# Optimization experiments

Measured on AMD Instinct MI355X. Metric: run time of the kernel, lower is better.

Reference implementation:

```python
import jax, jax.numpy as jnp
import numpy as np

N = 50000
E = 800000
IN_DIM = 128
HID = 64
HEADS = 4
OUT_DIM = 121
NEG_SLOPE = 0.2
EPS = 1e-16


def setup_inputs() -> dict:
    key = jax.random.key(0)
    ks = jax.random.split(key, 16)
    glorot = lambda k, shape: jax.random.normal(k, shape, jnp.float32) * (2.0 / (shape[0] + shape[-1])) ** 0.5
    HC = HEADS * HID
    return {
        "x": jax.random.normal(ks[0], (N, IN_DIM), jnp.float32),
        "edge_index": jax.random.randint(ks[1], (2, E), 0, N, jnp.int64),
        # conv1: GATConv(IN_DIM -> HID, heads=HEADS, concat)
        "W1": glorot(ks[2], (IN_DIM, HC)),
        "att_src1": glorot(ks[3], (HEADS, HID)),
        "att_dst1": glorot(ks[4], (HEADS, HID)),
        "b1": jnp.zeros((HC,), jnp.float32),
        # conv2: GATConv(HC -> HID, heads=HEADS, concat)
        "W2": glorot(ks[5], (HC, HC)),
        "att_src2": glorot(ks[6], (HEADS, HID)),
        "att_dst2": glorot(ks[7], (HEADS, HID)),
        "b2": jnp.zeros((HC,), jnp.float32),
        # post_mp: Linear(HC, HID) -> Dropout -> Linear(HID, OUT_DIM)
        "Wm1": glorot(ks[8], (HC, HID)),
        "bm1": jnp.zeros((HID,), jnp.float32),
        "Wm2": glorot(ks[9], (HID, OUT_DIM)),
        "bm2": jnp.zeros((OUT_DIM,), jnp.float32),
    }


def gat_conv(x, src, dst, W, att_src, att_dst, b):
    """PyG GATConv (concat=True, add_self_loops already applied to src/dst)."""
    n = x.shape[0]
    h = (x @ W).reshape(n, HEADS, -1)                     # [N, H, C]
    a_s = jnp.einsum("nhc,hc->nh", h, att_src)            # [N, H]
    a_d = jnp.einsum("nhc,hc->nh", h, att_dst)            # [N, H]
    e = jax.nn.leaky_relu(a_s[src] + a_d[dst], NEG_SLOPE)  # [Etot, H]
    # segment softmax over destination nodes
    m = jax.ops.segment_max(e, dst, num_segments=n)       # [N, H]
    ex = jnp.exp(e - m[dst])
    denom = jax.ops.segment_sum(ex, dst, num_segments=n)  # [N, H]
    alpha = ex / (denom[dst] + EPS)                        # [Etot, H]
    out = jax.ops.segment_sum(alpha[:, :, None] * h[src], dst, num_segments=n)  # [N, H, C]
    return out.reshape(n, -1) + b


def reference(x, edge_index, W1, att_src1, att_dst1, b1, W2, att_src2, att_dst2, b2, Wm1, bm1, Wm2, bm2):
    n = x.shape[0]
    loops = jnp.arange(n, dtype=edge_index.dtype)
    src = jnp.concatenate([edge_index[0], loops])
    dst = jnp.concatenate([edge_index[1], loops])
    h = jax.nn.relu(gat_conv(x, src, dst, W1, att_src1, att_dst1, b1))
    h = jax.nn.relu(gat_conv(h, src, dst, W2, att_src2, att_dst2, b2))
    h = h @ Wm1 + bm1
    h = h @ Wm2 + bm2
    return jax.nn.sigmoid(h)
```

## Files before the change

kernel.cpp:

```cpp
#include <hip/hip_runtime.h>
#include <hip/hip_bf16.h>
#include <float.h>

#define HEADS 4
#define HID 64
#define HC 256
#define NEG_SLOPE 0.2f
#define EPS 1e-16f
#define SLOG 7
#define SLOTS 128

typedef short bf16x8 __attribute__((ext_vector_type(8)));
typedef float f32x4 __attribute__((ext_vector_type(4)));
typedef unsigned short ushort8 __attribute__((ext_vector_type(8)));

__device__ __forceinline__ float bflo(unsigned u) { return __uint_as_float(u << 16); }
__device__ __forceinline__ float bfhi(unsigned u) { return __uint_as_float(u & 0xffff0000u); }
__device__ __forceinline__ unsigned packbf2(float a, float b) {
  __hip_bfloat16 ha = __float2bfloat16(a), hb = __float2bfloat16(b);
  unsigned short ua = *reinterpret_cast<unsigned short*>(&ha);
  unsigned short ub = *reinterpret_cast<unsigned short*>(&hb);
  return (unsigned)ua | ((unsigned)ub << 16);
}

#define PK 40

__global__ void __launch_bounds__(256) conv_gemm_attn(
    const __hip_bfloat16* __restrict__ A, const __hip_bfloat16* __restrict__ Bt,
    __hip_bfloat16* __restrict__ Cb,
    const float* __restrict__ att_s, const float* __restrict__ att_d,
    float* __restrict__ a_s, float* __restrict__ a_d,
    float* __restrict__ blockmax, int M, int K) {
  __shared__ unsigned short As[2][64 * PK];
  __shared__ unsigned short Bs[2][256 * PK];
  int tid = threadIdx.x;
  int lane = tid & 63, w = tid >> 6;
  int col16 = lane & 15, quad = lane >> 4;
  int row0 = blockIdx.x * 64;
  const unsigned short* Ag = (const unsigned short*)A;
  const unsigned short* Bg = (const unsigned short*)Bt;

  int ar = tid >> 2;
  int ako = (tid & 3) << 3;
  int agr = row0 + ar; if (agr >= M) agr = M - 1;
  const unsigned short* aga = Ag + (size_t)agr * K + ako;

  f32x4 acc[4][4] = {};
  int niter = K >> 5;

  ushort8 pa, pb[4];
  pa = *(const ushort8*)(aga);
#pragma unroll
  for (int p = 0; p < 4; p++) {
    int i2 = tid + (p << 8);
    int br = i2 >> 2, bko = (i2 & 3) << 3;
    pb[p] = *(const ushort8*)(Bg + (size_t)br * K + bko);
  }
  *(ushort8*)(&As[0][ar * PK + ako]) = pa;
#pragma unroll
  for (int p = 0; p < 4; p++) {
    int i2 = tid + (p << 8);
    int br = i2 >> 2, bko = (i2 & 3) << 3;
    *(ushort8*)(&Bs[0][br * PK + bko]) = pb[p];
  }
  __syncthreads();

  for (int it = 0; it < niter; ++it) {
    int cur = it & 1, nxt = cur ^ 1;
    int k1 = (it + 1) << 5;
    if (it + 1 < niter) {
      pa = *(const ushort8*)(aga + k1);
#pragma unroll
      for (int p = 0; p < 4; p++) {
        int i2 = tid + (p << 8);
        int br = i2 >> 2, bko = (i2 & 3) << 3;
        pb[p] = *(const ushort8*)(Bg + (size_t)br * K + k1 + bko);
      }
    }
    bf16x8 a[4], b[4];
#pragma unroll
    for (int i = 0; i < 4; i++)
      a[i] = *(const bf16x8*)(&As[cur][(i * 16 + col16) * PK + quad * 8]);
#pragma unroll
    for (int j = 0; j < 4; j++)
      b[j] = *(const bf16x8*)(&Bs[cur][((w << 6) + j * 16 + col16) * PK + quad * 8]);
#pragma unroll
    for (int i = 0; i < 4; i++)
#pragma unroll
      for (int j = 0; j < 4; j++)
        acc[i][j] = __builtin_amdgcn_mfma_f32_16x16x32_bf16(a[i], b[j], acc[i][j], 0, 0, 0);
    if (it + 1 < niter) {
      *(ushort8*)(&As[nxt][ar * PK + ako]) = pa;
#pragma unroll
      for (int p = 0; p < 4; p++) {
        int i2 = tid + (p << 8);
        int br = i2 >> 2, bko = (i2 & 3) << 3;
        *(ushort8*)(&Bs[nxt][br * PK + bko]) = pb[p];
      }
    }
    __syncthreads();
  }

#pragma unroll
  for (int i = 0; i < 4; i++) {
#pragma unroll
    for (int j = 0; j < 4; j++) {
      int gc = (w << 6) + j * 16 + col16;
      int grb = row0 + i * 16 + quad * 4;
#pragma unroll
      for (int r = 0; r < 4; r++) {
        int gr = grb + r;
        if (gr < M) Cb[(size_t)gr * 256 + gc] = __float2bfloat16(acc[i][j][r]);
      }
    }
  }

  float ws4[4], wd4[4];
#pragma unroll
  for (int j = 0; j < 4; j++) {
    ws4[j] = att_s[(w << 6) + j * 16 + col16];
    wd4[j] = att_d[(w << 6) + j * 16 + col16];
  }
  float wavemax = -FLT_MAX;
#pragma unroll
  for (int i = 0; i < 4; i++) {
#pragma unroll
    for (int r = 0; r < 4; r++) {
      float vs = 0.f, vd = 0.f;
#pragma unroll
      for (int j = 0; j < 4; j++) {
        vs += acc[i][j][r] * ws4[j];
        vd += acc[i][j][r] * wd4[j];
      }
#pragma unroll
      for (int off = 1; off < 16; off <<= 1) {
        vs += __shfl_xor(vs, off);
        vd += __shfl_xor(vd, off);
      }
      int gr = row0 + i * 16 + quad * 4 + r;
      if (col16 == 0 && gr < M) {
        a_s[(size_t)gr * 4 + w] = vs;
        a_d[(size_t)gr * 4 + w] = vd;
      }
      wavemax = fmaxf(wavemax, vs);
    }
  }
  wavemax = fmaxf(wavemax, __shfl_xor(wavemax, 16));
  wavemax = fmaxf(wavemax, __shfl_xor(wavemax, 32));
  if (lane == 0) blockmax[(size_t)blockIdx.x * 4 + w] = wavemax;
}

__global__ void __launch_bounds__(256) reduce_gmax(const float* __restrict__ blockmax,
                                                   float* __restrict__ gmaxf, int goff, int nb) {
  __shared__ float wm[4][4];
  int tid = threadIdx.x, lane = tid & 63, w = tid >> 6;
  int hd = tid & 3;
  float m = -FLT_MAX;
  for (int i = tid >> 2; i < nb; i += 64)
    m = fmaxf(m, blockmax[(size_t)i * 4 + hd]);
#pragma unroll
  for (int off = 4; off < 64; off <<= 1)
    m = fmaxf(m, __shfl_xor(m, off));
  if (lane < 4) wm[w][lane] = m;
  __syncthreads();
  if (tid < 4) {
    float r = fmaxf(fmaxf(wm[0][tid], wm[1][tid]), fmaxf(wm[2][tid], wm[3][tid]));
    gmaxf[goff + tid] = r;
  }
}

#define TS 72

__global__ void __launch_bounds__(256) postmp_fused(
    const __hip_bfloat16* __restrict__ A, const __hip_bfloat16* __restrict__ Wm1t,
    const __hip_bfloat16* __restrict__ Wm2t, const float* __restrict__ bm1,
    const float* __restrict__ bm2, float* __restrict__ out, int M) {
  __shared__ unsigned short smem[24576];
  unsigned short* W2s = &smem[15360];
  int tid = threadIdx.x;
  int lane = tid & 63, w = tid >> 6;
  int col16 = lane & 15, quad = lane >> 4;
  int row0 = blockIdx.x * 128;
  const unsigned short* Ag = (const unsigned short*)A;
  const unsigned short* Bg = (const unsigned short*)Wm1t;
  const unsigned short* W2g = (const unsigned short*)Wm2t;

#pragma unroll
  for (int c = tid; c < 1024; c += 256) {
    int r = c >> 3, ko = (c & 7) << 3;
    ushort8 v = {};
    if (r < 121) v = *(const ushort8*)(W2g + (size_t)r * 64 + ko);
    *(ushort8*)(&W2s[r * TS + ko]) = v;
  }

  int ar0 = tid >> 2, ako = (tid & 3) << 3;
  int agr0 = row0 + ar0;       if (agr0 >= M) agr0 = M - 1;
  int agr1 = row0 + ar0 + 64;  if (agr1 >= M) agr1 = M - 1;
  const unsigned short* aga0 = Ag + (size_t)agr0 * 256 + ako;
  const unsigned short* aga1 = Ag + (size_t)agr1 * 256 + ako;
  int br = tid >> 2, bko = (tid & 3) << 3;
  const unsigned short* bga = Bg + (size_t)br * 256 + bko;

  f32x4 acc1[2][4] = {};
  ushort8 pa0, pa1, pbv;
  pa0 = *(const ushort8*)(aga0);
  pa1 = *(const ushort8*)(aga1);
  pbv = *(const ushort8*)(bga);
  *(ushort8*)(&smem[ar0 * PK + ako]) = pa0;
  *(ushort8*)(&smem[(ar0 + 64) * PK + ako]) = pa1;
  *(ushort8*)(&smem[10240 + br * PK + bko]) = pbv;
  __syncthreads();

  for (int it = 0; it < 8; ++it) {
    int cur = it & 1, nxt = cur ^ 1;
    unsigned short* Asc = &smem[cur * 5120];
    unsigned short* Bsc = &smem[10240 + cur * 2560];
    int k1 = (it + 1) << 5;
    if (it + 1 < 8) {
      pa0 = *(const ushort8*)(aga0 + k1);
      pa1 = *(const ushort8*)(aga1 + k1);
      pbv = *(const ushort8*)(bga + k1);
    }
    bf16x8 a[2], b[4];
#pragma unroll
    for (int i = 0; i < 2; i++)
      a[i] = *(const bf16x8*)(&Asc[(w * 32 + i * 16 + col16) * PK + quad * 8]);
#pragma unroll
    for (int j = 0; j < 4; j++)
      b[j] = *(const bf16x8*)(&Bsc[(j * 16 + col16) * PK + quad * 8]);
#pragma unroll
    for (int i = 0; i < 2; i++)
#pragma unroll
      for (int j = 0; j < 4; j++)
        acc1[i][j] = __builtin_amdgcn_mfma_f32_16x16x32_bf16(a[i], b[j], acc1[i][j], 0, 0, 0);
    if (it + 1 < 8) {
      unsigned short* Asn = &smem[nxt * 5120];
      unsigned short* Bsn = &smem[10240 + nxt * 2560];
      *(ushort8*)(&Asn[ar0 * PK + ako]) = pa0;
      *(ushort8*)(&Asn[(ar0 + 64) * PK + ako]) = pa1;
      *(ushort8*)(&Bsn[br * PK + bko]) = pbv;
    }
    __syncthreads();
  }

  unsigned short* T = &smem[0];
#pragma unroll
  for (int i = 0; i < 2; i++) {
#pragma unroll
    for (int j = 0; j < 4; j++) {
      int col = j * 16 + col16;
      float bv = bm1[col];
#pragma unroll
      for (int r = 0; r < 4; r++) {
        int rl = w * 32 + i * 16 + quad * 4 + r;
        __hip_bfloat16 hv = __float2bfloat16(acc1[i][j][r] + bv);
        T[rl * TS + col] = *reinterpret_cast<unsigned short*>(&hv);
      }
    }
  }
  __syncthreads();

  int wm2 = w & 1, wn2 = w >> 1;
  f32x4 acc2[4][4] = {};
#pragma unroll
  for (int kk = 0; kk < 2; kk++) {
    bf16x8 a[4], b[4];
#pragma unroll
    for (int i = 0; i < 4; i++)
      a[i] = *(const bf16x8*)(&T[(wm2 * 64 + i * 16 + col16) * TS + kk * 32 + quad * 8]);
#pragma unroll
    for (int j = 0; j < 4; j++)
      b[j] = *(const bf16x8*)(&W2s[(wn2 * 64 + j * 16 + col16) * TS + kk * 32 + quad * 8]);
#pragma unroll
    for (int i = 0; i < 4; i++)
#pragma unroll
      for (int j = 0; j < 4; j++)
        acc2[i][j] = __builtin_amdgcn_mfma_f32_16x16x32_bf16(a[i], b[j], acc2[i][j], 0, 0, 0);
  }
#pragma unroll
  for (int i = 0; i < 4; i++) {
#pragma unroll
    for (int j = 0; j < 4; j++) {
      int gc = wn2 * 64 + j * 16 + col16;
      if (gc >= 121) continue;
      float bv = bm2[gc];
      int grb = row0 + wm2 * 64 + i * 16 + quad * 4;
#pragma unroll
      for (int r = 0; r < 4; r++) {
        int gr = grb + r;
        if (gr >= M) continue;
        float v = acc2[i][j][r] + bv;
        out[(size_t)gr * 121 + gc] = 1.f / (1.f + __expf(-v));
      }
    }
  }
}

__global__ void setup_all(const float* __restrict__ x, __hip_bfloat16* __restrict__ xb,
                          const float* __restrict__ W1, const float* __restrict__ W2,
                          const float* __restrict__ Wm1, const float* __restrict__ Wm2,
                          __hip_bfloat16* __restrict__ W1t, __hip_bfloat16* __restrict__ W2t,
                          __hip_bfloat16* __restrict__ Wm1t, __hip_bfloat16* __restrict__ Wm2t,
                          int* __restrict__ cur, int* __restrict__ slots,
                          int n, int castBlocks, int prepBlocks) {
  int b = blockIdx.x;
  int tid = threadIdx.x;
  if (b < castBlocks) {
    int i = b * 256 + tid;
    if (i < n * 32) {
      float4 v = *(const float4*)(x + 4 * (size_t)i);
      uint2 pk;
      pk.x = packbf2(v.x, v.y);
      pk.y = packbf2(v.z, v.w);
      *(uint2*)((unsigned*)xb + 2 * (size_t)i) = pk;
    }
    return;
  }
  b -= castBlocks;
  if (b < prepBlocks) {
    int i = b * 256 + tid;
    if (i < 128 * 256) {
      int nn = i / 128, kk = i - nn * 128;
      W1t[i] = __float2bfloat16(W1[(size_t)kk * 256 + nn]);
      return;
    }
    i -= 128 * 256;
    if (i < 256 * 256) {
      int nn = i / 256, kk = i - nn * 256;
      W2t[i] = __float2bfloat16(W2[(size_t)kk * 256 + nn]);
      return;
    }
    i -= 256 * 256;
    if (i < 256 * 64) {
      int nn = i / 256, kk = i - nn * 256;
      Wm1t[i] = __float2bfloat16(Wm1[(size_t)kk * 64 + nn]);
      return;
    }
    i -= 256 * 64;
    if (i < 64 * 121) {
      int nn = i / 64, kk = i - nn * 64;
      Wm2t[i] = __float2bfloat16(Wm2[(size_t)kk * 121 + nn]);
    }
    return;
  }
  b -= prepBlocks;
  {
    int i = b * 256 + tid;
    if (i < n) {
      cur[i] = 1;
      slots[(size_t)i << SLOG] = i;
    }
  }
}

__global__ void slot_fill(const int* __restrict__ ei, int E,
                          int* __restrict__ cur, int* __restrict__ slots) {
  int i = blockIdx.x * 256 + threadIdx.x;
  if (i >= E) return;
  int s = ei[i], d = ei[E + i];
  int pos = atomicAdd(&cur[d], 1);
  slots[((size_t)d << SLOG) + pos] = s;
}

__global__ void __launch_bounds__(256) gat_aggregate(
    const __hip_bfloat16* __restrict__ hb, const float* __restrict__ a_src,
    const float* __restrict__ a_dst, const int* __restrict__ cnt_arr,
    const int* __restrict__ slots, const float* __restrict__ bias,
    const float* __restrict__ gmaxf, int goff,
    __hip_bfloat16* __restrict__ out, int n) {
  __shared__ float plds[4][256];
  int wid = threadIdx.x >> 6;
  int lane = threadIdx.x & 63;
  int half = lane >> 5;
  int l32 = lane & 31;
  int qh = l32 >> 3;
  int node = (blockIdx.x << 2) + wid;
  if (node >= n) return;
  float4 adv = *(const float4*)(a_dst + (size_t)node * 4);
  float m0 = gmaxf[goff + 0] + adv.x; m0 = fmaxf(m0, NEG_SLOPE * m0);
  float m1 = gmaxf[goff + 1] + adv.y; m1 = fmaxf(m1, NEG_SLOPE * m1);
  float m2 = gmaxf[goff + 2] + adv.z; m2 = fmaxf(m2, NEG_SLOPE * m2);
  float m3 = gmaxf[goff + 3] + adv.w; m3 = fmaxf(m3, NEG_SLOPE * m3);
  int cntN = __builtin_amdgcn_readfirstlane(cnt_arr[node]);
  int beg = node << SLOG;
  const uint4* hw4 = (const uint4*)hb;

  float lq = 0.f;
  float c0 = 0.f, c1 = 0.f, c2 = 0.f, c3 = 0.f;
  float c4 = 0.f, c5 = 0.f, c6 = 0.f, c7 = 0.f;

  for (int cbeg = 0; cbeg < cntN; cbeg += 64) {
    int cnt = cntN - cbeg; if (cnt > 64) cnt = 64;
    int eidx = beg + cbeg + (lane < cnt ? lane : cnt - 1);
    int s_l = slots[eidx];
    float4 as = *(const float4*)(a_src + (size_t)s_l * 4);
    float v0 = as.x + adv.x; v0 = fmaxf(v0, NEG_SLOPE * v0);
    float v1 = as.y + adv.y; v1 = fmaxf(v1, NEG_SLOPE * v1);
    float v2 = as.z + adv.z; v2 = fmaxf(v2, NEG_SLOPE * v2);
    float v3 = as.w + adv.w; v3 = fmaxf(v3, NEG_SLOPE * v3);
    float p0 = __expf(v0 - m0), p1 = __expf(v1 - m1);
    float p2 = __expf(v2 - m2), p3 = __expf(v3 - m3);
    *(float4*)&plds[wid][lane * 4] = make_float4(p0, p1, p2, p3);
    __builtin_amdgcn_s_waitcnt(0);

    auto step = [&](int j) {
      int jj = j + half;
      bool dup = jj >= cnt;
      int jc = dup ? cnt - 1 : jj;
      int sj = __shfl(s_l, jc);
      float pq = plds[wid][jc * 4 + qh];
      if (dup) pq = 0.f;
      uint4 d = hw4[(size_t)sj * 32 + l32];
      c0 += pq * bflo(d.x); c1 += pq * bfhi(d.x);
      c2 += pq * bflo(d.y); c3 += pq * bfhi(d.y);
      c4 += pq * bflo(d.z); c5 += pq * bfhi(d.z);
      c6 += pq * bflo(d.w); c7 += pq * bfhi(d.w);
      lq += pq;
    };
    int j = 0;
    for (; j + 8 <= cnt; j += 8) { step(j); step(j + 2); step(j + 4); step(j + 6); }
    for (; j < cnt; j += 2) step(j);
  }

  lq += __shfl_xor(lq, 32);
  c0 += __shfl_xor(c0, 32); c1 += __shfl_xor(c1, 32);
  c2 += __shfl_xor(c2, 32); c3 += __shfl_xor(c3, 32);
  c4 += __shfl_xor(c4, 32); c5 += __shfl_xor(c5, 32);
  c6 += __shfl_xor(c6, 32); c7 += __shfl_xor(c7, 32);

  if (half == 0) {
    float4 bA = *(const float4*)(bias + 8 * l32);
    float4 bB = *(const float4*)(bias + 8 * l32 + 4);
    float rq = 1.f / (lq + EPS);
    float o0 = fmaxf(c0 * rq + bA.x, 0.f);
    float o1 = fmaxf(c1 * rq + bA.y, 0.f);
    float o2 = fmaxf(c2 * rq + bA.z, 0.f);
    float o3 = fmaxf(c3 * rq + bA.w, 0.f);
    float o4 = fmaxf(c4 * rq + bB.x, 0.f);
    float o5 = fmaxf(c5 * rq + bB.y, 0.f);
    float o6 = fmaxf(c6 * rq + bB.z, 0.f);
    float o7 = fmaxf(c7 * rq + bB.w, 0.f);
    uint4 pk;
    pk.x = packbf2(o0, o1);
    pk.y = packbf2(o2, o3);
    pk.z = packbf2(o4, o5);
    pk.w = packbf2(o6, o7);
    *(uint4*)((unsigned*)out + (size_t)node * 128 + l32 * 4) = pk;
  }
}

extern "C" void kernel_launch(void* const* d_in, const int* in_sizes, int n_in,
                              void* d_out, int out_size, void* d_ws, size_t ws_size,
                              hipStream_t stream) {
  const float* x      = (const float*)d_in[0];
  const int*   ei     = (const int*)d_in[1];
  const float* W1     = (const float*)d_in[2];
  const float* att_s1 = (const float*)d_in[3];
  const float* att_d1 = (const float*)d_in[4];
  const float* b1     = (const float*)d_in[5];
  const float* W2     = (const float*)d_in[6];
  const float* att_s2 = (const float*)d_in[7];
  const float* att_d2 = (const float*)d_in[8];
  const float* b2     = (const float*)d_in[9];
  const float* Wm1    = (const float*)d_in[10];
  const float* bm1    = (const float*)d_in[11];
  const float* Wm2    = (const float*)d_in[12];
  const float* bm2    = (const float*)d_in[13];
  float* out = (float*)d_out;

  int n = in_sizes[0] / 128;
  int E = in_sizes[1] / 2;

  char* ws = (char*)d_ws;
  size_t off = 0;
  auto carve = [&](size_t bytes) {
    char* p = ws + off;
    off += (bytes + 255) & ~(size_t)255;
    return p;
  };
  __hip_bfloat16* hb   = (__hip_bfloat16*)carve((size_t)n * HC * 2);
  __hip_bfloat16* aggb = (__hip_bfloat16*)carve((size_t)n * HC * 2);
  __hip_bfloat16* xb   = (__hip_bfloat16*)carve((size_t)n * 128 * 2);
  __hip_bfloat16* W1t  = (__hip_bfloat16*)carve((size_t)128 * HC * 2);
  __hip_bfloat16* W2t  = (__hip_bfloat16*)carve((size_t)HC * HC * 2);
  __hip_bfloat16* Wm1t = (__hip_bfloat16*)carve((size_t)HC * HID * 2);
  __hip_bfloat16* Wm2t = (__hip_bfloat16*)carve((size_t)HID * 121 * 2);
  float* as    = (float*)carve((size_t)n * HEADS * 4);
  float* ad    = (float*)carve((size_t)n * HEADS * 4);
  int*   cur   = (int*)carve((size_t)n * 4);
  int*   slots = (int*)carve(((size_t)n << SLOG) * 4);
  float* blockmax = (float*)carve((size_t)((n + 63) / 64) * 4 * 4);
  float* gmaxf    = (float*)carve((size_t)8 * 4);
  (void)ws_size;

  int rows64 = (n + 63) / 64;
  int castBlocks = (n * 32 + 255) / 256;
  int prepBlocks = (122432 + 255) / 256;
  int slotBlocks = (n + 255) / 256;

  setup_all<<<castBlocks + prepBlocks + slotBlocks, 256, 0, stream>>>(
      x, xb, W1, W2, Wm1, Wm2, W1t, W2t, Wm1t, Wm2t, cur, slots,
      n, castBlocks, prepBlocks);
  slot_fill<<<(E + 255) / 256, 256, 0, stream>>>(ei, E, cur, slots);

  conv_gemm_attn<<<rows64, 256, 0, stream>>>(
      xb, W1t, hb, att_s1, att_d1, as, ad, blockmax, n, 128);
  reduce_gmax<<<1, 256, 0, stream>>>(blockmax, gmaxf, 0, rows64);
  gat_aggregate<<<(n + 3) / 4, 256, 0, stream>>>(hb, as, ad, cur, slots, b1, gmaxf, 0, aggb, n);

  conv_gemm_attn<<<rows64, 256, 0, stream>>>(
      aggb, W2t, hb, att_s2, att_d2, as, ad, blockmax, n, HC);
  reduce_gmax<<<1, 256, 0, stream>>>(blockmax, gmaxf, 4, rows64);
  gat_aggregate<<<(n + 3) / 4, 256, 0, stream>>>(hb, as, ad, cur, slots, b2, gmaxf, 4, aggb, n);

  postmp_fused<<<(n + 127) / 128, 256, 0, stream>>>(aggb, Wm1t, Wm2t, bm1, bm2, out, n);
}
```

Baseline: 363.2 us.

## Fuse fp32-to-bf16 input cast into GEMM and drop LDS staging

```diff
diff --git a/kernel.cpp b/kernel.cpp
--- a/kernel.cpp
+++ b/kernel.cpp
@@ -25,80 +25,85 @@
 
 #define PK 40
 
+template <bool AF32, int K>
+__device__ __forceinline__ void load_afrag(const void* A, int row, int k, bf16x8& out) {
+  if (AF32) {
+    const float* p = (const float*)A + (size_t)row * K + k;
+    float4 u = *(const float4*)p;
+    float4 v = *(const float4*)(p + 4);
+    union { unsigned u4[4]; bf16x8 b; } cv;
+    cv.u4[0] = packbf2(u.x, u.y);
+    cv.u4[1] = packbf2(u.z, u.w);
+    cv.u4[2] = packbf2(v.x, v.y);
+    cv.u4[3] = packbf2(v.z, v.w);
+    out = cv.b;
+  } else {
+    out = *(const bf16x8*)((const unsigned short*)A + (size_t)row * K + k);
+  }
+}
+
+template <bool AF32, int K>
 __global__ void __launch_bounds__(256) conv_gemm_attn(
-    const __hip_bfloat16* __restrict__ A, const __hip_bfloat16* __restrict__ Bt,
+    const void* __restrict__ A, const __hip_bfloat16* __restrict__ Bt,
     __hip_bfloat16* __restrict__ Cb,
     const float* __restrict__ att_s, const float* __restrict__ att_d,
     float* __restrict__ a_s, float* __restrict__ a_d,
-    float* __restrict__ blockmax, int M, int K) {
-  __shared__ unsigned short As[2][64 * PK];
-  __shared__ unsigned short Bs[2][256 * PK];
+    float* __restrict__ blockmax, int M) {
   int tid = threadIdx.x;
   int lane = tid & 63, w = tid >> 6;
   int col16 = lane & 15, quad = lane >> 4;
   int row0 = blockIdx.x * 64;
-  const unsigned short* Ag = (const unsigned short*)A;
   const unsigned short* Bg = (const unsigned short*)Bt;
 
-  int ar = tid >> 2;
-  int ako = (tid & 3) << 3;
-  int agr = row0 + ar; if (agr >= M) agr = M - 1;
-  const unsigned short* aga = Ag + (size_t)agr * K + ako;
+  int arow[4], brow[4];
+#pragma unroll
+  for (int i = 0; i < 4; i++) {
+    int r = row0 + i * 16 + col16;
+    arow[i] = (r < M) ? r : (M - 1);
+    brow[i] = (w << 6) + i * 16 + col16;
+  }
+  int kq = quad << 3;
 
   f32x4 acc[4][4] = {};
-  int niter = K >> 5;
-
-  ushort8 pa, pb[4];
-  pa = *(const ushort8*)(aga);
-#pragma unroll
-  for (int p = 0; p < 4; p++) {
-    int i2 = tid + (p << 8);
-    int br = i2 >> 2, bko = (i2 & 3) << 3;
-    pb[p] = *(const ushort8*)(Bg + (size_t)br * K + bko);
-  }
-  *(ushort8*)(&As[0][ar * PK + ako]) = pa;
-#pragma unroll
-  for (int p = 0; p < 4; p++) {
-    int i2 = tid + (p << 8);
-    int br = i2 >> 2, bko = (i2 & 3) << 3;
-    *(ushort8*)(&Bs[0][br * PK + bko]) = pb[p];
-  }
-  __syncthreads();
-
-  for (int it = 0; it < niter; ++it) {
-    int cur = it & 1, nxt = cur ^ 1;
-    int k1 = (it + 1) << 5;
-    if (it + 1 < niter) {
-      pa = *(const ushort8*)(aga + k1);
-#pragma unroll
-      for (int p = 0; p < 4; p++) {
-        int i2 = tid + (p << 8);
-        int br = i2 >> 2, bko = (i2 & 3) << 3;
-        pb[p] = *(const ushort8*)(Bg + (size_t)br * K + k1 + bko);
-      }
-    }
-    bf16x8 a[4], b[4];
-#pragma unroll
-    for (int i = 0; i < 4; i++)
-      a[i] = *(const bf16x8*)(&As[cur][(i * 16 + col16) * PK + quad * 8]);
-#pragma unroll
-    for (int j = 0; j < 4; j++)
-      b[j] = *(const bf16x8*)(&Bs[cur][((w << 6) + j * 16 + col16) * PK + quad * 8]);
-#pragma unroll
-    for (int i = 0; i < 4; i++)
-#pragma unroll
-      for (int j = 0; j < 4; j++)
-        acc[i][j] = __builtin_amdgcn_mfma_f32_16x16x32_bf16(a[i], b[j], acc[i][j], 0, 0, 0);
-    if (it + 1 < niter) {
-      *(ushort8*)(&As[nxt][ar * PK + ako]) = pa;
-#pragma unroll
-      for (int p = 0; p < 4; p++) {
-        int i2 = tid + (p << 8);
-        int br = i2 >> 2, bko = (i2 & 3) << 3;
-        *(ushort8*)(&Bs[nxt][br * PK + bko]) = pb[p];
-      }
-    }
-    __syncthreads();
+  constexpr int NITER = K >> 5;
+
+  bf16x8 a0[4], b0[4], a1[4], b1[4];
+#pragma unroll
+  for (int i = 0; i < 4; i++) {
+    load_afrag<AF32, K>(A, arow[i], kq, a0[i]);
+    b0[i] = *(const bf16x8*)(Bg + (size_t)brow[i] * K + kq);
+  }
+
+#pragma unroll
+  for (int it = 0; it < NITER; ++it) {
+    int k1 = ((it + 1) << 5) + kq;
+    if ((it & 1) == 0) {
+      if (it + 1 < NITER) {
+#pragma unroll
+        for (int i = 0; i < 4; i++) {
+          load_afrag<AF32, K>(A, arow[i], k1, a1[i]);
+          b1[i] = *(const bf16x8*)(Bg + (size_t)brow[i] * K + k1);
+        }
+      }
+#pragma unroll
+      for (int i = 0; i < 4; i++)
+#pragma unroll
+        for (int j = 0; j < 4; j++)
+          acc[i][j] = __builtin_amdgcn_mfma_f32_16x16x32_bf16(a0[i], b0[j], acc[i][j], 0, 0, 0);
+    } else {
+      if (it + 1 < NITER) {
+#pragma unroll
+        for (int i = 0; i < 4; i++) {
+          load_afrag<AF32, K>(A, arow[i], k1, a0[i]);
+          b0[i] = *(const bf16x8*)(Bg + (size_t)brow[i] * K + k1);
+        }
+      }
+#pragma unroll
+      for (int i = 0; i < 4; i++)
+#pragma unroll
+        for (int j = 0; j < 4; j++)
+          acc[i][j] = __builtin_amdgcn_mfma_f32_16x16x32_bf16(a1[i], b1[j], acc[i][j], 0, 0, 0);
+    }
   }
 
 #pragma unroll
@@ -296,27 +301,14 @@
   }
 }
 
-__global__ void setup_all(const float* __restrict__ x, __hip_bfloat16* __restrict__ xb,
-                          const float* __restrict__ W1, const float* __restrict__ W2,
+__global__ void setup_all(const float* __restrict__ W1, const float* __restrict__ W2,
                           const float* __restrict__ Wm1, const float* __restrict__ Wm2,
                           __hip_bfloat16* __restrict__ W1t, __hip_bfloat16* __restrict__ W2t,
                           __hip_bfloat16* __restrict__ Wm1t, __hip_bfloat16* __restrict__ Wm2t,
                           int* __restrict__ cur, int* __restrict__ slots,
-                          int n, int castBlocks, int prepBlocks) {
+                          int n, int prepBlocks) {
   int b = blockIdx.x;
   int tid = threadIdx.x;
-  if (b < castBlocks) {
-    int i = b * 256 + tid;
-    if (i < n * 32) {
-      float4 v = *(const float4*)(x + 4 * (size_t)i);
-      uint2 pk;
-      pk.x = packbf2(v.x, v.y);
-      pk.y = packbf2(v.z, v.w);
-      *(uint2*)((unsigned*)xb + 2 * (size_t)i) = pk;
-    }
-    return;
-  }
-  b -= castBlocks;
   if (b < prepBlocks) {
     int i = b * 256 + tid;
     if (i < 128 * 256) {
@@ -480,7 +472,6 @@
   };
   __hip_bfloat16* hb   = (__hip_bfloat16*)carve((size_t)n * HC * 2);
   __hip_bfloat16* aggb = (__hip_bfloat16*)carve((size_t)n * HC * 2);
-  __hip_bfloat16* xb   = (__hip_bfloat16*)carve((size_t)n * 128 * 2);
   __hip_bfloat16* W1t  = (__hip_bfloat16*)carve((size_t)128 * HC * 2);
   __hip_bfloat16* W2t  = (__hip_bfloat16*)carve((size_t)HC * HC * 2);
   __hip_bfloat16* Wm1t = (__hip_bfloat16*)carve((size_t)HC * HID * 2);
@@ -494,22 +485,20 @@
   (void)ws_size;
 
   int rows64 = (n + 63) / 64;
-  int castBlocks = (n * 32 + 255) / 256;
   int prepBlocks = (122432 + 255) / 256;
   int slotBlocks = (n + 255) / 256;
 
-  setup_all<<<castBlocks + prepBlocks + slotBlocks, 256, 0, stream>>>(
-      x, xb, W1, W2, Wm1, Wm2, W1t, W2t, Wm1t, Wm2t, cur, slots,
-      n, castBlocks, prepBlocks);
+  setup_all<<<prepBlocks + slotBlocks, 256, 0, stream>>>(
+      W1, W2, Wm1, Wm2, W1t, W2t, Wm1t, Wm2t, cur, slots, n, prepBlocks);
   slot_fill<<<(E + 255) / 256, 256, 0, stream>>>(ei, E, cur, slots);
 
-  conv_gemm_attn<<<rows64, 256, 0, stream>>>(
-      xb, W1t, hb, att_s1, att_d1, as, ad, blockmax, n, 128);
+  conv_gemm_attn<true, 128><<<rows64, 256, 0, stream>>>(
+      x, W1t, hb, att_s1, att_d1, as, ad, blockmax, n);
   reduce_gmax<<<1, 256, 0, stream>>>(blockmax, gmaxf, 0, rows64);
   gat_aggregate<<<(n + 3) / 4, 256, 0, stream>>>(hb, as, ad, cur, slots, b1, gmaxf, 0, aggb, n);
 
-  conv_gemm_attn<<<rows64, 256, 0, stream>>>(
-      aggb, W2t, hb, att_s2, att_d2, as, ad, blockmax, n, HC);
+  conv_gemm_attn<false, 256><<<rows64, 256, 0, stream>>>(
+      aggb, W2t, hb, att_s2, att_d2, as, ad, blockmax, n);
   reduce_gmax<<<1, 256, 0, stream>>>(blockmax, gmaxf, 4, rows64);
   gat_aggregate<<<(n + 3) / 4, 256, 0, stream>>>(hb, as, ad, cur, slots, b2, gmaxf, 4, aggb, n);
 
```

Result: slower. 388.9 us (+7.1%).
